# Kernel tuning notes

Measured on AMD Instinct MI355X. Metric: run time of the kernel, lower is better.

## Reference

```python
import jax, jax.numpy as jnp
import numpy as np
import math

N_HEADS = 8
INPUT_DIM = 512
EMBED_DIM = 512
KEY_DIM = EMBED_DIM // N_HEADS  # 64, also val_dim
BATCH = 16
GRAPH = 1024


def setup_inputs() -> dict:
    key = jax.random.key(0)
    ks = jax.random.split(key, 10)
    def uinit(k, shape):
        stdv = 1.0 / math.sqrt(shape[-1])
        return jax.random.uniform(k, shape, jnp.float32, -stdv, stdv)
    return {
        "h_node_in": jax.random.normal(ks[0], (BATCH, GRAPH, INPUT_DIM), jnp.float32),
        "h_pos_in": jax.random.normal(ks[1], (BATCH, GRAPH, INPUT_DIM), jnp.float32),
        "W_query_node": uinit(ks[2], (N_HEADS, INPUT_DIM, KEY_DIM)),
        "W_query_pos": uinit(ks[3], (N_HEADS, INPUT_DIM, KEY_DIM)),
        "W_key_node": uinit(ks[4], (N_HEADS, INPUT_DIM, KEY_DIM)),
        "W_key_pos": uinit(ks[5], (N_HEADS, INPUT_DIM, KEY_DIM)),
        "W_val_node": uinit(ks[6], (2 * N_HEADS, INPUT_DIM, KEY_DIM)),
        "W_val_pos": uinit(ks[7], (2 * N_HEADS, INPUT_DIM, KEY_DIM)),
        "W_out_node": uinit(ks[8], (N_HEADS, 2 * KEY_DIM, EMBED_DIM)),
        "W_out_pos": uinit(ks[9], (N_HEADS, 2 * KEY_DIM, EMBED_DIM)),
    }


def reference(h_node_in, h_pos_in, W_query_node, W_query_pos, W_key_node,
              W_key_pos, W_val_node, W_val_pos, W_out_node, W_out_pos):
    norm = 1.0 / math.sqrt(KEY_DIM)
    H = N_HEADS
    # projections: [B,N,D] x [H,D,k] -> [H,B,N,k]
    Q_node = jnp.einsum('bnd,hdk->hbnk', h_node_in, W_query_node)
    Q_pos = jnp.einsum('bnd,hdk->hbnk', h_pos_in, W_query_pos)
    K_node = jnp.einsum('bnd,hdk->hbnk', h_node_in, W_key_node)
    K_pos = jnp.einsum('bnd,hdk->hbnk', h_pos_in, W_key_pos)
    # values: [2H,D,v] -> (2,H,B,N,v)
    V_node = jnp.einsum('bnd,hdv->hbnv', h_node_in, W_val_node).reshape(2, H, *h_node_in.shape[:2], KEY_DIM)
    V_pos = jnp.einsum('bnd,hdv->hbnv', h_pos_in, W_val_pos).reshape(2, H, *h_pos_in.shape[:2], KEY_DIM)
    # two shared softmax attentions: [H,B,Nq,Nk]
    attn1 = jax.nn.softmax(norm * jnp.einsum('hbqk,hbnk->hbqn', Q_node, K_node), axis=-1)
    attn2 = jax.nn.softmax(norm * jnp.einsum('hbqk,hbnk->hbqn', Q_pos, K_pos), axis=-1)
    heads_node = jnp.concatenate([
        jnp.einsum('hbqn,hbnv->hbqv', attn1, V_node[0]),
        jnp.einsum('hbqn,hbnv->hbqv', attn2, V_node[1])], axis=-1)  # [H,B,N,2v]
    heads_pos = jnp.concatenate([
        jnp.einsum('hbqn,hbnv->hbqv', attn1, V_pos[0]),
        jnp.einsum('hbqn,hbnv->hbqv', attn2, V_pos[1])], axis=-1)
    # per-head output GEMM, summed over heads: [H,B,N,2v] x [H,2v,E] -> [B,N,E]
    out_node = jnp.einsum('hbnc,hce->bne', heads_node, W_out_node)
    out_pos = jnp.einsum('hbnc,hce->bne', heads_pos, W_out_pos)
    return (out_node, out_pos)
```

## Files before the change

### kernel.cpp

```cpp
#include <hip/hip_runtime.h>
#include <hip/hip_bf16.h>
#include <stdint.h>

typedef __attribute__((ext_vector_type(8))) short short8;
typedef __attribute__((ext_vector_type(4))) short short4_t;
typedef __attribute__((ext_vector_type(4))) float f32x4;
typedef __attribute__((ext_vector_type(16))) float f32x16;
typedef __attribute__((ext_vector_type(4))) unsigned uint4v;

#define DEVFN static __device__ __forceinline__

constexpr int BATCH = 16;
constexpr int GRAPH = 1024;
constexpr int IDIM  = 512;
constexpr int EDIM  = 512;
constexpr int NH    = 8;
constexpr int KD    = 64;
constexpr int TOK   = BATCH * GRAPH;
constexpr int QKC   = 1024;
constexpr int HC    = 1024;
constexpr float SMSCALE = 0.125f * 1.44269504088896340736f;

DEVFN unsigned short f2bf(float x) {
    union { float f; unsigned u; } v; v.f = x;
    unsigned r = v.u + 0x7fffu + ((v.u >> 16) & 1u);
    return (unsigned short)(r >> 16);
}

DEVFN unsigned cvtpk(float a, float b) {
    unsigned r;
    asm("v_cvt_pk_bf16_f32 %0, %1, %2" : "=v"(r) : "v"(a), "v"(b));
    return r;
}

DEVFN void plswap(unsigned &x, unsigned &y) {
    asm("v_permlane32_swap_b32 %0, %1" : "+v"(x), "+v"(y));
}

DEVFN void load16(const void* g, void* l) {
    __builtin_amdgcn_global_load_lds(
        (const __attribute__((address_space(1))) void*)g,
        (__attribute__((address_space(3))) void*)l, 16, 0, 0);
}

__global__ __launch_bounds__(256) void cvt_x_kernel(const float4* __restrict__ x0,
                                                    const float4* __restrict__ x1,
                                                    short4_t* __restrict__ y0,
                                                    short4_t* __restrict__ y1) {
    const float4* x = blockIdx.y ? x1 : x0;
    short4_t*     y = blockIdx.y ? y1 : y0;
    const int i = blockIdx.x * 256 + threadIdx.x;
    const float4 v = x[i];
    short4_t o;
    o[0] = (short)f2bf(v.x); o[1] = (short)f2bf(v.y);
    o[2] = (short)f2bf(v.z); o[3] = (short)f2bf(v.w);
    y[i] = o;
}

__global__ __launch_bounds__(256)
void pack_w_kernel(const float* __restrict__ Wqn, const float* __restrict__ Wkn,
                   const float* __restrict__ Wvn,
                   const float* __restrict__ Wqp, const float* __restrict__ Wkp,
                   const float* __restrict__ Wvp,
                   const float* __restrict__ Won, const float* __restrict__ Wop,
                   unsigned short* __restrict__ Wn, unsigned short* __restrict__ Wp2,
                   unsigned short* __restrict__ WoN, unsigned short* __restrict__ WoP)
{
    __shared__ float T[64][65];
    const int bid = blockIdx.x, tid = threadIdx.x;

    const float* src; unsigned short* dst;
    int sld, dld; size_t sbase, dbase;
    float scale = 1.f;

    if (bid < 512) {
        const int st = bid >> 8, t = bid & 255;
        const int tr = t >> 3, tc = t & 7;
        dst = st ? Wp2 : Wn;
        int head;
        if (tr < 8)       { src = st ? Wqp : Wqn; head = tr;      scale = SMSCALE; }
        else if (tr < 16) { src = st ? Wkp : Wkn; head = tr - 8; }
        else              { src = st ? Wvp : Wvn; head = tr - 16; }
        sld = 64; dld = 512;
        sbase = (size_t)(head * 512 + tc * 64) * 64;
        dbase = (size_t)(tr * 64) * 512 + tc * 64;
    } else {
        const int b2 = bid - 512;
        const int st = b2 >> 7, t = b2 & 127;
        const int tr = t >> 4, tc = t & 15;
        src = st ? Wop : Won;
        dst = st ? WoP : WoN;
        sld = 512; dld = 1024;
        sbase = (size_t)(tc * 64) * 512 + tr * 64;
        dbase = (size_t)(tr * 64) * 1024 + tc * 64;
    }

    {
        const int j = tid & 63, i0 = tid >> 6;
        #pragma unroll
        for (int p = 0; p < 16; ++p) {
            const int i = p * 4 + i0;
            T[i][j] = src[sbase + (size_t)i * sld + j];
        }
    }
    __syncthreads();
    {
        const int i = tid & 63, j0 = tid >> 6;
        #pragma unroll
        for (int p = 0; p < 16; ++p) {
            const int j = p * 4 + j0;
            dst[dbase + (size_t)j * dld + i] = f2bf(T[i][j] * scale);
        }
    }
}

template<int K, bool VSPLIT, typename OutT>
__global__ __launch_bounds__(256)
void gemm_bt_kernel(const unsigned short* __restrict__ A0, const unsigned short* __restrict__ A1,
                    const unsigned short* __restrict__ B0, const unsigned short* __restrict__ B1,
                    OutT* __restrict__ C0, OutT* __restrict__ C1,
                    unsigned short* __restrict__ V0, unsigned short* __restrict__ V1,
                    int ldc)
{
    __shared__ unsigned short As[128 * 64];
    __shared__ unsigned short Bs[128 * 64];
    const unsigned short* A  = blockIdx.z ? A1 : A0;
    const unsigned short* Bt = blockIdx.z ? B1 : B0;

    const int tid = threadIdx.x, wave = tid >> 6, lane = tid & 63;
    const int g = lane >> 4, ln = lane & 15;
    const int m0 = blockIdx.x * 128, n0 = blockIdx.y * 128;
    const int wr = (wave >> 1) * 64, wc = (wave & 1) * 64;

    f32x4 acc[4][4] = {};

    for (int k0 = 0; k0 < K; k0 += 64) {
        #pragma unroll
        for (int j = 0; j < 4; ++j) {
            const int c = (wave * 4 + j) * 64 + lane;
            const int row = c >> 3;
            const int col = ((c & 7) ^ (row & 7)) * 8;
            load16(A  + (size_t)(m0 + row) * K + k0 + col, (char*)As + c * 16);
            load16(Bt + (size_t)(n0 + row) * K + k0 + col, (char*)Bs + c * 16);
        }
        __syncthreads();
        #pragma unroll
        for (int kk = 0; kk < 2; ++kk) {
            short8 af[4], bfr[4];
            #pragma unroll
            for (int i = 0; i < 4; ++i) {
                const int ra = wr + i * 16 + ln;
                af[i]  = *(const short8*)((const char*)As + ra * 128 + (((kk * 4 + g) ^ (ra & 7)) * 16));
                const int rb = wc + i * 16 + ln;
                bfr[i] = *(const short8*)((const char*)Bs + rb * 128 + (((kk * 4 + g) ^ (rb & 7)) * 16));
            }
            #pragma unroll
            for (int mi = 0; mi < 4; ++mi)
                #pragma unroll
                for (int ni = 0; ni < 4; ++ni)
                    acc[mi][ni] = __builtin_amdgcn_mfma_f32_16x16x32_bf16(af[mi], bfr[ni], acc[mi][ni], 0, 0, 0);
        }
        __syncthreads();
    }

    if (!VSPLIT || n0 < 1024) {
        OutT* C = blockIdx.z ? C1 : C0;
        #pragma unroll
        for (int mi = 0; mi < 4; ++mi)
            #pragma unroll
            for (int ni = 0; ni < 4; ++ni)
                #pragma unroll
                for (int r = 0; r < 4; ++r) {
                    const size_t m = (size_t)(m0 + wr + mi * 16 + g * 4 + r);
                    const size_t n = (size_t)(n0 + wc + ni * 16 + ln);
                    if constexpr (sizeof(OutT) == 4) C[m * ldc + n] = acc[mi][ni][r];
                    else                             C[m * ldc + n] = (OutT)f2bf(acc[mi][ni][r]);
                }
    } else {
        unsigned short* Vt = blockIdx.z ? V1 : V0;
        #pragma unroll
        for (int mi = 0; mi < 4; ++mi)
            #pragma unroll
            for (int ni = 0; ni < 4; ++ni) {
                uint2 w;
                w.x = cvtpk(acc[mi][ni][0], acc[mi][ni][1]);
                w.y = cvtpk(acc[mi][ni][2], acc[mi][ni][3]);
                const size_t vrow = (size_t)(n0 - 1024 + wc + ni * 16 + ln);
                const size_t mcol = (size_t)(m0 + wr + mi * 16 + g * 4);
                *(uint2*)(Vt + vrow * TOK + mcol) = w;
            }
    }
}

__global__ __launch_bounds__(256, 2)
void attn_kernel(const unsigned short* __restrict__ projn,
                 const unsigned short* __restrict__ projp,
                 const unsigned short* __restrict__ Vtn,
                 const unsigned short* __restrict__ Vtp,
                 unsigned short* __restrict__ headsn,
                 unsigned short* __restrict__ headsp)
{
    __shared__ unsigned short Kl[2][64 * 64];
    __shared__ unsigned short Vl[2][128 * 64];

    const int bid  = blockIdx.x;
    const int slot = bid >> 3;
    const int g    = (bid & 7) * 32 + (slot >> 2);
    const int qt   = slot & 3;
    const int a    = (g & 15) >> 3, h = g & 7;
    const int b    = g >> 4;

    const int tid = threadIdx.x, wave = tid >> 6, lane = tid & 63;
    const int q = lane & 31, hi = lane >> 5;

    const unsigned short* proj = a ? projp : projn;
    const int tok0 = b * GRAPH;
    const size_t qrow0 = (size_t)(tok0 + qt * 256 + wave * 64 + q);
    const int qc  = h * KD;
    const int kc  = IDIM + h * KD;
    const int vr0 = (a * NH + h) * KD;

    short8 qf[2][4];
    #pragma unroll
    for (int qi = 0; qi < 2; ++qi)
        #pragma unroll
        for (int ds = 0; ds < 4; ++ds)
            qf[qi][ds] = *(const short8*)(proj + (qrow0 + qi * 32) * QKC + qc + ds * 16 + hi * 8);

    const char* kap[2]; int kds[2];
    #pragma unroll
    for (int j = 0; j < 2; ++j) {
        const int c = (wave * 2 + j) * 64 + lane;
        const int row = c >> 3;
        const int col = ((c & 7) ^ (row & 7)) * 8;
        kap[j] = (const char*)(proj + (size_t)(tok0 + row) * QKC + kc + col);
        kds[j] = c * 16;
    }
    const char* vap[4]; int vds[4];
    #pragma unroll
    for (int j = 0; j < 4; ++j) {
        const int c = (wave * 4 + j) * 64 + lane;
        const int row = c >> 3;
        const int col = ((c & 7) ^ (row & 7)) * 8;
        const unsigned short* base = (row < 64)
            ? (Vtn + (size_t)(vr0 + row) * TOK)
            : (Vtp + (size_t)(vr0 + row - 64) * TOK);
        vap[j] = (const char*)(base + tok0 + col);
        vds[j] = c * 16;
    }

    auto stage = [&](int bb) {
        #pragma unroll
        for (int j = 0; j < 2; ++j) { load16(kap[j], (char*)Kl[bb] + kds[j]); kap[j] += (size_t)64 * QKC * 2; }
        #pragma unroll
        for (int j = 0; j < 4; ++j) { load16(vap[j], (char*)Vl[bb] + vds[j]); vap[j] += 64 * 2; }
    };

    f32x16 oacc[2][4] = {};
    float l_run[2] = {0.f, 0.f};

    stage(0);
    __syncthreads();

    for (int kt = 0; kt < 16; ++kt) {
        const int bb = kt & 1;
        if (kt < 15) stage(bb ^ 1);

        short8 pfrag[2][4];
        #pragma unroll
        for (int kb = 0; kb < 2; ++kb) {
            f32x16 s0 = {}, s1 = {};
            __builtin_amdgcn_s_setprio(1);
            #pragma unroll
            for (int ds = 0; ds < 4; ++ds) {
                const int row = kb * 32 + q;
                const short8 kf = *(const short8*)((const char*)Kl[bb] + row * 128 + (((ds * 2 + hi) ^ (row & 7)) * 16));
                s0 = __builtin_amdgcn_mfma_f32_32x32x16_bf16(kf, qf[0][ds], s0, 0, 0, 0);
                s1 = __builtin_amdgcn_mfma_f32_32x32x16_bf16(kf, qf[1][ds], s1, 0, 0, 0);
            }
            __builtin_amdgcn_s_setprio(0);

            float ps0 = 0.f, ps1 = 0.f;
            #pragma unroll
            for (int r = 0; r < 16; ++r) {
                const float p0 = __builtin_amdgcn_exp2f(s0[r]); s0[r] = p0; ps0 += p0;
                const float p1 = __builtin_amdgcn_exp2f(s1[r]); s1[r] = p1; ps1 += p1;
            }
            l_run[0] += ps0; l_run[1] += ps1;

            #pragma unroll
            for (int sh = 0; sh < 2; ++sh) {
                const int s = kb * 2 + sh, o = 8 * sh;
                {
                    unsigned A0 = cvtpk(s0[o + 0], s0[o + 1]);
                    unsigned A1 = cvtpk(s0[o + 2], s0[o + 3]);
                    unsigned B0 = cvtpk(s0[o + 4], s0[o + 5]);
                    unsigned B1 = cvtpk(s0[o + 6], s0[o + 7]);
                    plswap(A0, B0); plswap(A1, B1);
                    uint4v pw; pw[0] = A0; pw[1] = A1; pw[2] = B0; pw[3] = B1;
                    pfrag[0][s] = __builtin_bit_cast(short8, pw);
                }
                {
                    unsigned A0 = cvtpk(s1[o + 0], s1[o + 1]);
                    unsigned A1 = cvtpk(s1[o + 2], s1[o + 3]);
                    unsigned B0 = cvtpk(s1[o + 4], s1[o + 5]);
                    unsigned B1 = cvtpk(s1[o + 6], s1[o + 7]);
                    plswap(A0, B0); plswap(A1, B1);
                    uint4v pw; pw[0] = A0; pw[1] = A1; pw[2] = B0; pw[3] = B1;
                    pfrag[1][s] = __builtin_bit_cast(short8, pw);
                }
            }
        }

        __builtin_amdgcn_s_setprio(1);
        #pragma unroll
        for (int s = 0; s < 4; ++s) {
            #pragma unroll
            for (int vb = 0; vb < 4; ++vb) {
                const int row = vb * 32 + q;
                const short8 vf = *(const short8*)((const char*)Vl[bb] + row * 128 + (((s * 2 + hi) ^ (row & 7)) * 16));
                oacc[0][vb] = __builtin_amdgcn_mfma_f32_32x32x16_bf16(vf, pfrag[0][s], oacc[0][vb], 0, 0, 0);
                oacc[1][vb] = __builtin_amdgcn_mfma_f32_32x32x16_bf16(vf, pfrag[1][s], oacc[1][vb], 0, 0, 0);
            }
        }
        __builtin_amdgcn_s_setprio(0);
        __syncthreads();
    }

    #pragma unroll
    for (int qi = 0; qi < 2; ++qi) {
        l_run[qi] += __shfl_xor(l_run[qi], 32);
        const float inv = 1.0f / l_run[qi];
        const size_t qrow = qrow0 + qi * 32;
        #pragma unroll
        for (int vb = 0; vb < 4; ++vb) {
            unsigned short* heads = (vb < 2) ? headsn : headsp;
            const int colbase = h * 128 + a * 64 + (vb & 1) * 32;
            #pragma unroll
            for (int w = 0; w < 8; ++w) {
                const unsigned pk = cvtpk(oacc[qi][vb][2 * w] * inv, oacc[qi][vb][2 * w + 1] * inv);
                const int v = ((2 * w) & 3) + 8 * (w >> 1) + 4 * hi;
                *(unsigned*)(heads + qrow * HC + colbase + v) = pk;
            }
        }
    }
}

extern "C" void kernel_launch(void* const* d_in, const int* in_sizes, int n_in,
                              void* d_out, int out_size, void* d_ws, size_t ws_size,
                              hipStream_t stream)
{
    const float* hn  = (const float*)d_in[0];
    const float* hp  = (const float*)d_in[1];
    const float* Wqn = (const float*)d_in[2];
    const float* Wqp = (const float*)d_in[3];
    const float* Wkn = (const float*)d_in[4];
    const float* Wkp = (const float*)d_in[5];
    const float* Wvn = (const float*)d_in[6];
    const float* Wvp = (const float*)d_in[7];
    const float* Won = (const float*)d_in[8];
    const float* Wop = (const float*)d_in[9];
    float* out = (float*)d_out;

    char* ws = (char*)d_ws;
    size_t off = 0;
    auto take = [&](size_t nbytes) -> char* {
        char* p = ws + off;
        off += (nbytes + 255) & ~(size_t)255;
        return p;
    };
    unsigned short* Xn  = (unsigned short*)take((size_t)TOK * IDIM * 2);
    unsigned short* Xp  = (unsigned short*)take((size_t)TOK * IDIM * 2);
    unsigned short* Wn  = (unsigned short*)take((size_t)2048 * 512 * 2);
    unsigned short* Wp  = (unsigned short*)take((size_t)2048 * 512 * 2);
    unsigned short* WoN = (unsigned short*)take((size_t)512 * 1024 * 2);
    unsigned short* WoP = (unsigned short*)take((size_t)512 * 1024 * 2);
    unsigned short* Pn  = (unsigned short*)take((size_t)TOK * QKC * 2);
    unsigned short* Pp  = (unsigned short*)take((size_t)TOK * QKC * 2);
    unsigned short* Vtn = (unsigned short*)take((size_t)1024 * TOK * 2);
    unsigned short* Vtp = (unsigned short*)take((size_t)1024 * TOK * 2);
    unsigned short* Hn  = (unsigned short*)take((size_t)TOK * HC * 2);
    unsigned short* Hp  = (unsigned short*)take((size_t)TOK * HC * 2);

    cvt_x_kernel<<<dim3(TOK * IDIM / 4 / 256, 2), 256, 0, stream>>>(
        (const float4*)hn, (const float4*)hp, (short4_t*)Xn, (short4_t*)Xp);
    pack_w_kernel<<<768, 256, 0, stream>>>(
        Wqn, Wkn, Wvn, Wqp, Wkp, Wvp, Won, Wop, Wn, Wp, WoN, WoP);

    gemm_bt_kernel<512, true, unsigned short><<<dim3(128, 16, 2), 256, 0, stream>>>(
        Xn, Xp, Wn, Wp, Pn, Pp, Vtn, Vtp, QKC);

    attn_kernel<<<1024, 256, 0, stream>>>(Pn, Pp, Vtn, Vtp, Hn, Hp);

    gemm_bt_kernel<1024, false, float><<<dim3(128, 4, 2), 256, 0, stream>>>(
        Hn, Hp, WoN, WoP, out, out + (size_t)TOK * EDIM,
        (unsigned short*)nullptr, (unsigned short*)nullptr, EDIM);
}
```

Measured before the change: 405.5 us.

## Use 256x256 double-buffered GEMM tiles with LDS-staged transposed V stores

Replaces the 128x128 single-buffered projection and output GEMMs with a 512-thread 256x256 tile kernel. It double-buffers LDS with async loads, using vmcnt waits and raw barriers so the next K-slice loads while MFMAs run. The transposed V output is staged through LDS so global writes become coalesced 16-byte rows. Larger tiles cut global traffic per FLOP, but they raise register and LDS pressure (128 KB shared per block) and produce fewer blocks, which may hurt occupancy or tail balance.

```diff
diff --git a/kernel.cpp b/kernel.cpp
--- a/kernel.cpp
+++ b/kernel.cpp
@@ -115,80 +115,133 @@
 }
 
 template<int K, bool VSPLIT, typename OutT>
-__global__ __launch_bounds__(256)
-void gemm_bt_kernel(const unsigned short* __restrict__ A0, const unsigned short* __restrict__ A1,
+__global__ __launch_bounds__(512, 2)
+void gemm256_kernel(const unsigned short* __restrict__ A0, const unsigned short* __restrict__ A1,
                     const unsigned short* __restrict__ B0, const unsigned short* __restrict__ B1,
                     OutT* __restrict__ C0, OutT* __restrict__ C1,
                     unsigned short* __restrict__ V0, unsigned short* __restrict__ V1,
                     int ldc)
 {
-    __shared__ unsigned short As[128 * 64];
-    __shared__ unsigned short Bs[128 * 64];
+    __shared__ __align__(16) unsigned short smem[2][2][256 * 64];
     const unsigned short* A  = blockIdx.z ? A1 : A0;
     const unsigned short* Bt = blockIdx.z ? B1 : B0;
 
-    const int tid = threadIdx.x, wave = tid >> 6, lane = tid & 63;
+    const int tid = threadIdx.x, lane = tid & 63;
+    const int wave = tid >> 6;
     const int g = lane >> 4, ln = lane & 15;
-    const int m0 = blockIdx.x * 128, n0 = blockIdx.y * 128;
-    const int wr = (wave >> 1) * 64, wc = (wave & 1) * 64;
-
-    f32x4 acc[4][4] = {};
-
-    for (int k0 = 0; k0 < K; k0 += 64) {
+    const int wm = wave >> 2, wn = wave & 3;
+    const int n0 = blockIdx.x * 256, m0 = blockIdx.y * 256;
+
+    const char* ap[4]; const char* bp[4];
+    #pragma unroll
+    for (int j = 0; j < 4; ++j) {
+        const int c = j * 512 + tid;
+        const int row = c >> 3;
+        const int colg = (c & 7) ^ (row & 7);
+        ap[j] = (const char*)(A  + (size_t)(m0 + row) * K + colg * 8);
+        bp[j] = (const char*)(Bt + (size_t)(n0 + row) * K + colg * 8);
+    }
+    auto stage = [&](int t, int bb) {
         #pragma unroll
         for (int j = 0; j < 4; ++j) {
-            const int c = (wave * 4 + j) * 64 + lane;
-            const int row = c >> 3;
-            const int col = ((c & 7) ^ (row & 7)) * 8;
-            load16(A  + (size_t)(m0 + row) * K + k0 + col, (char*)As + c * 16);
-            load16(Bt + (size_t)(n0 + row) * K + k0 + col, (char*)Bs + c * 16);
-        }
-        __syncthreads();
-        #pragma unroll
-        for (int kk = 0; kk < 2; ++kk) {
-            short8 af[4], bfr[4];
-            #pragma unroll
-            for (int i = 0; i < 4; ++i) {
-                const int ra = wr + i * 16 + ln;
-                af[i]  = *(const short8*)((const char*)As + ra * 128 + (((kk * 4 + g) ^ (ra & 7)) * 16));
-                const int rb = wc + i * 16 + ln;
-                bfr[i] = *(const short8*)((const char*)Bs + rb * 128 + (((kk * 4 + g) ^ (rb & 7)) * 16));
-            }
-            #pragma unroll
-            for (int mi = 0; mi < 4; ++mi)
-                #pragma unroll
-                for (int ni = 0; ni < 4; ++ni)
-                    acc[mi][ni] = __builtin_amdgcn_mfma_f32_16x16x32_bf16(af[mi], bfr[ni], acc[mi][ni], 0, 0, 0);
-        }
-        __syncthreads();
-    }
-
-    if (!VSPLIT || n0 < 1024) {
+            const int c = j * 512 + tid;
+            load16(ap[j] + t * 128, (char*)smem[bb][0] + c * 16);
+            load16(bp[j] + t * 128, (char*)smem[bb][1] + c * 16);
+        }
+    };
+
+    f32x4 acc[8][4] = {};
+    constexpr int NT = K / 64;
+
+    stage(0, 0);
+    for (int t = 0; t < NT; ++t) {
+        const int bb = t & 1;
+        if (t + 1 < NT) {
+            stage(t + 1, bb ^ 1);
+            asm volatile("s_waitcnt vmcnt(8)" ::: "memory");
+        } else {
+            asm volatile("s_waitcnt vmcnt(0)" ::: "memory");
+        }
+        __builtin_amdgcn_s_barrier();
+
+        const char* As = (const char*)smem[bb][0];
+        const char* Bs = (const char*)smem[bb][1];
+        short8 bfr[4][2];
+        #pragma unroll
+        for (int ni = 0; ni < 4; ++ni) {
+            const int rb = wn * 64 + ni * 16 + ln;
+            bfr[ni][0] = *(const short8*)(Bs + rb * 128 + ((g ^ (rb & 7)) * 16));
+            bfr[ni][1] = *(const short8*)(Bs + rb * 128 + (((4 + g) ^ (rb & 7)) * 16));
+        }
+        __builtin_amdgcn_s_setprio(1);
+        #pragma unroll
+        for (int mi = 0; mi < 8; ++mi) {
+            const int ra = wm * 128 + mi * 16 + ln;
+            const short8 a0 = *(const short8*)(As + ra * 128 + ((g ^ (ra & 7)) * 16));
+            const short8 a1 = *(const short8*)(As + ra * 128 + (((4 + g) ^ (ra & 7)) * 16));
+            #pragma unroll
+            for (int ni = 0; ni < 4; ++ni) {
+                acc[mi][ni] = __builtin_amdgcn_mfma_f32_16x16x32_bf16(a0, bfr[ni][0], acc[mi][ni], 0, 0, 0);
+                acc[mi][ni] = __builtin_amdgcn_mfma_f32_16x16x32_bf16(a1, bfr[ni][1], acc[mi][ni], 0, 0, 0);
+            }
+        }
+        __builtin_amdgcn_s_setprio(0);
+        __builtin_amdgcn_s_barrier();
+    }
+
+    if constexpr (!VSPLIT) {
         OutT* C = blockIdx.z ? C1 : C0;
         #pragma unroll
-        for (int mi = 0; mi < 4; ++mi)
+        for (int mi = 0; mi < 8; ++mi)
             #pragma unroll
             for (int ni = 0; ni < 4; ++ni)
                 #pragma unroll
                 for (int r = 0; r < 4; ++r) {
-                    const size_t m = (size_t)(m0 + wr + mi * 16 + g * 4 + r);
-                    const size_t n = (size_t)(n0 + wc + ni * 16 + ln);
-                    if constexpr (sizeof(OutT) == 4) C[m * ldc + n] = acc[mi][ni][r];
-                    else                             C[m * ldc + n] = (OutT)f2bf(acc[mi][ni][r]);
+                    const size_t m = (size_t)(m0 + wm * 128 + mi * 16 + g * 4 + r);
+                    const size_t n = (size_t)(n0 + wn * 64 + ni * 16 + ln);
+                    C[m * ldc + n] = acc[mi][ni][r];
+                }
+    } else if (n0 < 1024) {
+        unsigned short* C = (unsigned short*)(blockIdx.z ? C1 : C0);
+        #pragma unroll
+        for (int mi = 0; mi < 8; ++mi)
+            #pragma unroll
+            for (int ni = 0; ni < 4; ++ni)
+                #pragma unroll
+                for (int r = 0; r < 4; ++r) {
+                    const size_t m = (size_t)(m0 + wm * 128 + mi * 16 + g * 4 + r);
+                    const size_t n = (size_t)(n0 + wn * 64 + ni * 16 + ln);
+                    C[m * ldc + n] = f2bf(acc[mi][ni][r]);
                 }
     } else {
         unsigned short* Vt = blockIdx.z ? V1 : V0;
-        #pragma unroll
-        for (int mi = 0; mi < 4; ++mi)
-            #pragma unroll
-            for (int ni = 0; ni < 4; ++ni) {
-                uint2 w;
-                w.x = cvtpk(acc[mi][ni][0], acc[mi][ni][1]);
-                w.y = cvtpk(acc[mi][ni][2], acc[mi][ni][3]);
-                const size_t vrow = (size_t)(n0 - 1024 + wc + ni * 16 + ln);
-                const size_t mcol = (size_t)(m0 + wr + mi * 16 + g * 4);
-                *(uint2*)(Vt + vrow * TOK + mcol) = w;
-            }
+        unsigned short* Ts = &smem[0][0][0];
+        #pragma unroll
+        for (int mh = 0; mh < 2; ++mh) {
+            if (wm == mh) {
+                #pragma unroll
+                for (int mi = 0; mi < 8; ++mi) {
+                    const int mloc = mi * 16 + g * 4;
+                    #pragma unroll
+                    for (int ni = 0; ni < 4; ++ni) {
+                        const int nl = wn * 64 + ni * 16 + ln;
+                        uint2 w;
+                        w.x = cvtpk(acc[mi][ni][0], acc[mi][ni][1]);
+                        w.y = cvtpk(acc[mi][ni][2], acc[mi][ni][3]);
+                        *(uint2*)(Ts + nl * 136 + mloc) = w;
+                    }
+                }
+            }
+            __syncthreads();
+            #pragma unroll
+            for (int it = 0; it < 8; ++it) {
+                const int c = it * 512 + tid;
+                const int row = c >> 4, gr = c & 15;
+                *(short8*)(Vt + (size_t)(n0 - 1024 + row) * TOK + m0 + mh * 128 + gr * 8) =
+                    *(const short8*)(Ts + row * 136 + gr * 8);
+            }
+            __syncthreads();
+        }
     }
 }
 
@@ -387,12 +440,12 @@
     pack_w_kernel<<<768, 256, 0, stream>>>(
         Wqn, Wkn, Wvn, Wqp, Wkp, Wvp, Won, Wop, Wn, Wp, WoN, WoP);
 
-    gemm_bt_kernel<512, true, unsigned short><<<dim3(128, 16, 2), 256, 0, stream>>>(
+    gemm256_kernel<512, true, unsigned short><<<dim3(8, 64, 2), 512, 0, stream>>>(
         Xn, Xp, Wn, Wp, Pn, Pp, Vtn, Vtp, QKC);
 
     attn_kernel<<<1024, 256, 0, stream>>>(Pn, Pp, Vtn, Vtp, Hn, Hp);
 
-    gemm_bt_kernel<1024, false, float><<<dim3(128, 4, 2), 256, 0, stream>>>(
+    gemm256_kernel<1024, false, float><<<dim3(2, 64, 2), 512, 0, stream>>>(
         Hn, Hp, WoN, WoP, out, out + (size_t)TOK * EDIM,
         (unsigned short*)nullptr, (unsigned short*)nullptr, EDIM);
 }
```

New measurement: 373.5 us. 1.09x faster.

## Double-buffer GEMM LDS tiles and compute V-transpose as a separate swapped GEMM

Applied to the files above, without the earlier changes.

Rewrites the GEMM kernel to double-buffer A/B tiles in LDS, prefetching the next K-slice while MFMAs run on the current one. It uses manual vmcnt waits, raw barriers, wave priority hints and occupancy 2. The V-transposed projection is now its own GEMM with swapped operands (W_v as A, X as B), so its output is written row-major straight into Vt instead of through a strided transposed store. The block grid is reordered so n varies fastest. This costs an extra launch and doubles LDS use per block.

```diff
diff --git a/kernel.cpp b/kernel.cpp
--- a/kernel.cpp
+++ b/kernel.cpp
@@ -114,45 +114,66 @@
     }
 }
 
-template<int K, bool VSPLIT, typename OutT>
-__global__ __launch_bounds__(256)
-void gemm_bt_kernel(const unsigned short* __restrict__ A0, const unsigned short* __restrict__ A1,
+template<int K, typename OutT>
+__global__ __launch_bounds__(256, 2)
+void gemm128_kernel(const unsigned short* __restrict__ A0, const unsigned short* __restrict__ A1,
                     const unsigned short* __restrict__ B0, const unsigned short* __restrict__ B1,
                     OutT* __restrict__ C0, OutT* __restrict__ C1,
-                    unsigned short* __restrict__ V0, unsigned short* __restrict__ V1,
                     int ldc)
 {
-    __shared__ unsigned short As[128 * 64];
-    __shared__ unsigned short Bs[128 * 64];
+    __shared__ __align__(16) unsigned short smem[2][2][128 * 64];
     const unsigned short* A  = blockIdx.z ? A1 : A0;
     const unsigned short* Bt = blockIdx.z ? B1 : B0;
 
     const int tid = threadIdx.x, wave = tid >> 6, lane = tid & 63;
     const int g = lane >> 4, ln = lane & 15;
-    const int m0 = blockIdx.x * 128, n0 = blockIdx.y * 128;
+    const int n0 = blockIdx.x * 128, m0 = blockIdx.y * 128;
     const int wr = (wave >> 1) * 64, wc = (wave & 1) * 64;
 
+    const char* ap[4]; const char* bp[4];
+    #pragma unroll
+    for (int j = 0; j < 4; ++j) {
+        const int c = j * 256 + tid;
+        const int row = c >> 3;
+        const int colg = (c & 7) ^ (row & 7);
+        ap[j] = (const char*)(A  + (size_t)(m0 + row) * K + colg * 8);
+        bp[j] = (const char*)(Bt + (size_t)(n0 + row) * K + colg * 8);
+    }
+    auto stage = [&](int t, int bb) {
+        #pragma unroll
+        for (int j = 0; j < 4; ++j) {
+            const int c = j * 256 + tid;
+            load16(ap[j] + t * 128, (char*)smem[bb][0] + c * 16);
+            load16(bp[j] + t * 128, (char*)smem[bb][1] + c * 16);
+        }
+    };
+
     f32x4 acc[4][4] = {};
-
-    for (int k0 = 0; k0 < K; k0 += 64) {
-        #pragma unroll
-        for (int j = 0; j < 4; ++j) {
-            const int c = (wave * 4 + j) * 64 + lane;
-            const int row = c >> 3;
-            const int col = ((c & 7) ^ (row & 7)) * 8;
-            load16(A  + (size_t)(m0 + row) * K + k0 + col, (char*)As + c * 16);
-            load16(Bt + (size_t)(n0 + row) * K + k0 + col, (char*)Bs + c * 16);
-        }
-        __syncthreads();
+    constexpr int NT = K / 64;
+
+    stage(0, 0);
+    for (int t = 0; t < NT; ++t) {
+        const int bb = t & 1;
+        if (t + 1 < NT) {
+            stage(t + 1, bb ^ 1);
+            asm volatile("s_waitcnt vmcnt(8)" ::: "memory");
+        } else {
+            asm volatile("s_waitcnt vmcnt(0)" ::: "memory");
+        }
+        __builtin_amdgcn_s_barrier();
+
+        const char* As = (const char*)smem[bb][0];
+        const char* Bs = (const char*)smem[bb][1];
+        __builtin_amdgcn_s_setprio(1);
         #pragma unroll
         for (int kk = 0; kk < 2; ++kk) {
             short8 af[4], bfr[4];
             #pragma unroll
             for (int i = 0; i < 4; ++i) {
                 const int ra = wr + i * 16 + ln;
-                af[i]  = *(const short8*)((const char*)As + ra * 128 + (((kk * 4 + g) ^ (ra & 7)) * 16));
+                af[i]  = *(const short8*)(As + ra * 128 + (((kk * 4 + g) ^ (ra & 7)) * 16));
                 const int rb = wc + i * 16 + ln;
-                bfr[i] = *(const short8*)((const char*)Bs + rb * 128 + (((kk * 4 + g) ^ (rb & 7)) * 16));
+                bfr[i] = *(const short8*)(Bs + rb * 128 + (((kk * 4 + g) ^ (rb & 7)) * 16));
             }
             #pragma unroll
             for (int mi = 0; mi < 4; ++mi)
@@ -160,36 +181,22 @@
                 for (int ni = 0; ni < 4; ++ni)
                     acc[mi][ni] = __builtin_amdgcn_mfma_f32_16x16x32_bf16(af[mi], bfr[ni], acc[mi][ni], 0, 0, 0);
         }
-        __syncthreads();
-    }
-
-    if (!VSPLIT || n0 < 1024) {
-        OutT* C = blockIdx.z ? C1 : C0;
-        #pragma unroll
-        for (int mi = 0; mi < 4; ++mi)
-            #pragma unroll
-            for (int ni = 0; ni < 4; ++ni)
-                #pragma unroll
-                for (int r = 0; r < 4; ++r) {
-                    const size_t m = (size_t)(m0 + wr + mi * 16 + g * 4 + r);
-                    const size_t n = (size_t)(n0 + wc + ni * 16 + ln);
-                    if constexpr (sizeof(OutT) == 4) C[m * ldc + n] = acc[mi][ni][r];
-                    else                             C[m * ldc + n] = (OutT)f2bf(acc[mi][ni][r]);
-                }
-    } else {
-        unsigned short* Vt = blockIdx.z ? V1 : V0;
-        #pragma unroll
-        for (int mi = 0; mi < 4; ++mi)
-            #pragma unroll
-            for (int ni = 0; ni < 4; ++ni) {
-                uint2 w;
-                w.x = cvtpk(acc[mi][ni][0], acc[mi][ni][1]);
-                w.y = cvtpk(acc[mi][ni][2], acc[mi][ni][3]);
-                const size_t vrow = (size_t)(n0 - 1024 + wc + ni * 16 + ln);
-                const size_t mcol = (size_t)(m0 + wr + mi * 16 + g * 4);
-                *(uint2*)(Vt + vrow * TOK + mcol) = w;
-            }
-    }
+        __builtin_amdgcn_s_setprio(0);
+        __builtin_amdgcn_s_barrier();
+    }
+
+    OutT* C = blockIdx.z ? C1 : C0;
+    #pragma unroll
+    for (int mi = 0; mi < 4; ++mi)
+        #pragma unroll
+        for (int ni = 0; ni < 4; ++ni)
+            #pragma unroll
+            for (int r = 0; r < 4; ++r) {
+                const size_t m = (size_t)(m0 + wr + mi * 16 + g * 4 + r);
+                const size_t n = (size_t)(n0 + wc + ni * 16 + ln);
+                if constexpr (sizeof(OutT) == 4) C[m * ldc + n] = acc[mi][ni][r];
+                else                             C[m * ldc + n] = (OutT)f2bf(acc[mi][ni][r]);
+            }
 }
 
 __global__ __launch_bounds__(256, 2)
@@ -387,12 +394,14 @@
     pack_w_kernel<<<768, 256, 0, stream>>>(
         Wqn, Wkn, Wvn, Wqp, Wkp, Wvp, Won, Wop, Wn, Wp, WoN, WoP);
 
-    gemm_bt_kernel<512, true, unsigned short><<<dim3(128, 16, 2), 256, 0, stream>>>(
-        Xn, Xp, Wn, Wp, Pn, Pp, Vtn, Vtp, QKC);
+    gemm128_kernel<512, unsigned short><<<dim3(8, 128, 2), 256, 0, stream>>>(
+        Xn, Xp, Wn, Wp, Pn, Pp, QKC);
+
+    gemm128_kernel<512, unsigned short><<<dim3(128, 8, 2), 256, 0, stream>>>(
+        Wn + 1024 * 512, Wp + 1024 * 512, Xn, Xp, Vtn, Vtp, TOK);
 
     attn_kernel<<<1024, 256, 0, stream>>>(Pn, Pp, Vtn, Vtp, Hn, Hp);
 
-    gemm_bt_kernel<1024, false, float><<<dim3(128, 4, 2), 256, 0, stream>>>(
-        Hn, Hp, WoN, WoP, out, out + (size_t)TOK * EDIM,
-        (unsigned short*)nullptr, (unsigned short*)nullptr, EDIM);
-}
+    gemm128_kernel<1024, float><<<dim3(4, 128, 2), 256, 0, stream>>>(
+        Hn, Hp, WoN, WoP, out, out + (size_t)TOK * EDIM, EDIM);
+}
```

New measurement: 395.2 us. -2.5%, faster.
